# Kernel tuning notes

Measured on AMD Instinct MI355X. Metric: run time of the kernel, lower is better.

## Reference

```python
import jax, jax.numpy as jnp
import numpy as np


def setup_inputs() -> dict:
    key = jax.random.key(0)
    k1, k2 = jax.random.split(key)
    B, N, M, D = 16, 2048, 2048, 3
    predictions = jax.random.normal(k1, (B, N, D), dtype=jnp.float32)
    targets = jax.random.normal(k2, (B, M, D), dtype=jnp.float32)
    return {"predictions": predictions, "targets": targets}


def reference(predictions, targets):
    # Batched pairwise squared distances: [B, N, M]
    # d(i,j) = |x_i|^2 + |y_j|^2 - 2 x_i . y_j
    xx = jnp.sum(predictions * predictions, axis=-1)  # [B, N]
    yy = jnp.sum(targets * targets, axis=-1)          # [B, M]
    xy = jnp.einsum("bnd,bmd->bnm", predictions, targets)  # [B, N, M]
    P = xx[:, :, None] + yy[:, None, :] - 2.0 * xy    # [B, N, M]
    # Chamfer: sum of per-point nearest-neighbor squared distances, both directions
    loss = jnp.sum(jnp.min(P, axis=2)) + jnp.sum(jnp.min(P, axis=1))
    return loss
```

## Files before the change

kernel.cpp:

```cpp
#include <hip/hip_runtime.h>
#include <math.h>


#define BATCH   16
#define NPTS    2048
#define KSLICE  32
#define SLICE   64
#define SPT     8
#define NCOMBO  32
#define NBLK2   256

__global__ __launch_bounds__(256) void chamfer_partial(
    const float* __restrict__ preds,
    const float* __restrict__ tgts,
    float* __restrict__ partial,
    int* __restrict__ counter)
{
    __shared__ float4 q[SLICE];

    const int bid   = blockIdx.x;
    const int combo = bid & (NCOMBO - 1);
    const int slice = bid >> 5;
    const int dir   = combo >> 4;
    const int b     = combo & 15;

    if (bid == 0 && threadIdx.x == 0) *counter = 0;

    const float* src = (dir ? tgts : preds) + (size_t)b * NPTS * 3;
    const float* opp = (dir ? preds : tgts) + (size_t)b * NPTS * 3;

    if (threadIdx.x < SLICE) {
        const int jj = slice * SLICE + threadIdx.x;
        const float y0 = opp[3 * jj + 0];
        const float y1 = opp[3 * jj + 1];
        const float y2 = opp[3 * jj + 2];
        q[threadIdx.x] = make_float4(y0, y1, y2, y0 * y0 + y1 * y1 + y2 * y2);
    }

    float n0[SPT], n1[SPT], n2[SPT], m[SPT];
    #pragma unroll
    for (int k = 0; k < SPT; k++) {
        const int i = threadIdx.x + 256 * k;
        n0[k] = -2.0f * src[3 * i + 0];
        n1[k] = -2.0f * src[3 * i + 1];
        n2[k] = -2.0f * src[3 * i + 2];
        m[k]  = INFINITY;
    }
    __syncthreads();

    #pragma unroll 2
    for (int j = 0; j < SLICE; j++) {
        const float4 Q = q[j];
        #pragma unroll
        for (int k = 0; k < SPT; k++) {
            const float s = fmaf(n0[k], Q.x, fmaf(n1[k], Q.y, fmaf(n2[k], Q.z, Q.w)));
            m[k] = fminf(m[k], s);
        }
    }

    float* pp = partial + ((size_t)combo * KSLICE + slice) * NPTS;
    #pragma unroll
    for (int k = 0; k < SPT; k++)
        pp[threadIdx.x + 256 * k] = m[k];
}

__global__ __launch_bounds__(256) void chamfer_reduce(
    const float* __restrict__ preds,
    const float* __restrict__ tgts,
    const float* __restrict__ partial,
    float* __restrict__ blocksum,
    int* __restrict__ counter,
    float* __restrict__ out)
{
    __shared__ float wsum[4];
    __shared__ bool  amLast;

    const int idx   = blockIdx.x * 256 + threadIdx.x;
    const int combo = idx >> 11;
    const int i     = idx & (NPTS - 1);
    const int dir   = combo >> 4;
    const int b     = combo & 15;

    const float* src = (dir ? tgts : preds) + (size_t)b * NPTS * 3;
    const float x0 = src[3 * i + 0];
    const float x1 = src[3 * i + 1];
    const float x2 = src[3 * i + 2];
    const float xx = x0 * x0 + x1 * x1 + x2 * x2;

    const float* pp = partial + (size_t)combo * KSLICE * NPTS + i;
    float mn = pp[0];
    #pragma unroll
    for (int s = 1; s < KSLICE; s++)
        mn = fminf(mn, pp[(size_t)s * NPTS]);

    float val = xx + mn;

    #pragma unroll
    for (int off = 32; off > 0; off >>= 1)
        val += __shfl_down(val, off, 64);

    const int lane = threadIdx.x & 63;
    const int wid  = threadIdx.x >> 6;
    if (lane == 0) wsum[wid] = val;
    __syncthreads();

    if (threadIdx.x == 0) {
        const float bsum = wsum[0] + wsum[1] + wsum[2] + wsum[3];
        __hip_atomic_store(&blocksum[blockIdx.x], bsum,
                           __ATOMIC_RELAXED, __HIP_MEMORY_SCOPE_AGENT);
        __threadfence();
        amLast = (atomicAdd(counter, 1) == NBLK2 - 1);
    }
    __syncthreads();

    if (amLast) {
        __threadfence();
        float v = __hip_atomic_load(&blocksum[threadIdx.x],
                                    __ATOMIC_RELAXED, __HIP_MEMORY_SCOPE_AGENT);
        #pragma unroll
        for (int off = 32; off > 0; off >>= 1)
            v += __shfl_down(v, off, 64);
        if (lane == 0) wsum[wid] = v;
        __syncthreads();
        if (threadIdx.x == 0)
            out[0] = wsum[0] + wsum[1] + wsum[2] + wsum[3];
    }
}

extern "C" void kernel_launch(void* const* d_in, const int* in_sizes, int n_in,
                              void* d_out, int out_size, void* d_ws, size_t ws_size,
                              hipStream_t stream) {
    const float* preds = (const float*)d_in[0];
    const float* tgts  = (const float*)d_in[1];
    float* out      = (float*)d_out;
    float* partial  = (float*)d_ws;
    float* blocksum = partial + (size_t)NCOMBO * KSLICE * NPTS;
    int*   counter  = (int*)(blocksum + NBLK2);

    chamfer_partial<<<NCOMBO * KSLICE, 256, 0, stream>>>(preds, tgts, partial, counter);
    chamfer_reduce<<<NBLK2, 256, 0, stream>>>(preds, tgts, partial, blocksum, counter, out);
}
```

Measured before the change: 76.90 us.

## Use packed FMA over SoA target slices with two slices per block

```diff
diff --git a/kernel.cpp b/kernel.cpp
--- a/kernel.cpp
+++ b/kernel.cpp
@@ -2,66 +2,98 @@
 #include <math.h>
 
 
-#define BATCH   16
+typedef float v2f __attribute__((ext_vector_type(2)));
+
 #define NPTS    2048
+#define NCOMBO  32
 #define KSLICE  32
 #define SLICE   64
-#define SPT     8
-#define NCOMBO  32
+#define SPT     16
 #define NBLK2   256
 
-__global__ __launch_bounds__(256) void chamfer_partial(
+__device__ __forceinline__ v2f pkfma(v2f a, v2f b, v2f c) {
+#if __has_builtin(__builtin_elementwise_fma)
+    return __builtin_elementwise_fma(a, b, c);
+#else
+    v2f d; d.x = fmaf(a.x, b.x, c.x); d.y = fmaf(a.y, b.y, c.y); return d;
+#endif
+}
+
+__global__ __launch_bounds__(256, 2) void chamfer_partial(
     const float* __restrict__ preds,
     const float* __restrict__ tgts,
     float* __restrict__ partial,
     int* __restrict__ counter)
 {
-    __shared__ float4 q[SLICE];
+    __shared__ __align__(16) float qx[2][SLICE];
+    __shared__ __align__(16) float qy[2][SLICE];
+    __shared__ __align__(16) float qz[2][SLICE];
+    __shared__ __align__(16) float qw[2][SLICE];
 
     const int bid   = blockIdx.x;
     const int combo = bid & (NCOMBO - 1);
-    const int slice = bid >> 5;
+    const int spair = bid >> 5;
     const int dir   = combo >> 4;
     const int b     = combo & 15;
+
+    const int sb    = threadIdx.x >> 7;
+    const int tt    = threadIdx.x & 127;
+    const int slice = spair * 2 + sb;
 
     if (bid == 0 && threadIdx.x == 0) *counter = 0;
 
     const float* src = (dir ? tgts : preds) + (size_t)b * NPTS * 3;
     const float* opp = (dir ? preds : tgts) + (size_t)b * NPTS * 3;
 
-    if (threadIdx.x < SLICE) {
-        const int jj = slice * SLICE + threadIdx.x;
+    if (tt < SLICE) {
+        const int jj = slice * SLICE + tt;
         const float y0 = opp[3 * jj + 0];
         const float y1 = opp[3 * jj + 1];
         const float y2 = opp[3 * jj + 2];
-        q[threadIdx.x] = make_float4(y0, y1, y2, y0 * y0 + y1 * y1 + y2 * y2);
+        qx[sb][tt] = y0;
+        qy[sb][tt] = y1;
+        qz[sb][tt] = y2;
+        qw[sb][tt] = y0 * y0 + y1 * y1 + y2 * y2;
     }
 
-    float n0[SPT], n1[SPT], n2[SPT], m[SPT];
+    v2f nn0[SPT], nn1[SPT], nn2[SPT];
+    float m[SPT];
     #pragma unroll
     for (int k = 0; k < SPT; k++) {
-        const int i = threadIdx.x + 256 * k;
-        n0[k] = -2.0f * src[3 * i + 0];
-        n1[k] = -2.0f * src[3 * i + 1];
-        n2[k] = -2.0f * src[3 * i + 2];
-        m[k]  = INFINITY;
+        const int i = tt + 128 * k;
+        const float a0 = -2.0f * src[3 * i + 0];
+        const float a1 = -2.0f * src[3 * i + 1];
+        const float a2 = -2.0f * src[3 * i + 2];
+        nn0[k] = (v2f){a0, a0};
+        nn1[k] = (v2f){a1, a1};
+        nn2[k] = (v2f){a2, a2};
+        m[k]   = INFINITY;
     }
     __syncthreads();
 
     #pragma unroll 2
-    for (int j = 0; j < SLICE; j++) {
-        const float4 Q = q[j];
+    for (int jg = 0; jg < SLICE / 4; jg++) {
+        const float4 X = *(const float4*)&qx[sb][4 * jg];
+        const float4 Y = *(const float4*)&qy[sb][4 * jg];
+        const float4 Z = *(const float4*)&qz[sb][4 * jg];
+        const float4 W = *(const float4*)&qw[sb][4 * jg];
+        const v2f Xa = {X.x, X.y}, Xb = {X.z, X.w};
+        const v2f Ya = {Y.x, Y.y}, Yb = {Y.z, Y.w};
+        const v2f Za = {Z.x, Z.y}, Zb = {Z.z, Z.w};
+        const v2f Wa = {W.x, W.y}, Wb = {W.z, W.w};
         #pragma unroll
         for (int k = 0; k < SPT; k++) {
-            const float s = fmaf(n0[k], Q.x, fmaf(n1[k], Q.y, fmaf(n2[k], Q.z, Q.w)));
-            m[k] = fminf(m[k], s);
+            const v2f sa = pkfma(nn0[k], Xa, pkfma(nn1[k], Ya, pkfma(nn2[k], Za, Wa)));
+            m[k] = fminf(fminf(m[k], sa.x), sa.y);
+            const v2f sb2 = pkfma(nn0[k], Xb, pkfma(nn1[k], Yb, pkfma(nn2[k], Zb, Wb)));
+            m[k] = fminf(fminf(m[k], sb2.x), sb2.y);
         }
     }
 
     float* pp = partial + ((size_t)combo * KSLICE + slice) * NPTS;
     #pragma unroll
     for (int k = 0; k < SPT; k++)
-        pp[threadIdx.x + 256 * k] = m[k];
+        pp[tt + 128 * k] = m[k];
 }
 
 __global__ __launch_bounds__(256) void chamfer_reduce(
@@ -137,6 +169,6 @@
     float* blocksum = partial + (size_t)NCOMBO * KSLICE * NPTS;
     int*   counter  = (int*)(blocksum + NBLK2);
 
-    chamfer_partial<<<NCOMBO * KSLICE, 256, 0, stream>>>(preds, tgts, partial, counter);
+    chamfer_partial<<<NCOMBO * (KSLICE / 2), 256, 0, stream>>>(preds, tgts, partial, counter);
     chamfer_reduce<<<NBLK2, 256, 0, stream>>>(preds, tgts, partial, blocksum, counter, out);
 }
```

Result: no change. 77.06 us (+0.2%).
